# Optimization experiments

Hardware: AMD Instinct MI355X
Metric: run time of the kernel (lower is better)

## Reference

```python
import jax, jax.numpy as jnp
import numpy as np

B, S, D = 4, 1024, 1024
NH, HD = 16, 64            # heads, head_dim
R = 4                      # channel_shrink_ratio
LD, LHD = D // R, HD // R  # layout hidden, layout head_dim
MAXP = 2048                # max_position_embeddings


def _heads(x, nh, hd):
    # [B,S,nh*hd] -> [B,nh,S,hd]
    b, s, _ = x.shape
    return x.reshape(b, s, nh, hd).transpose(0, 2, 1, 3)


def setup_inputs() -> dict:
    key = jax.random.key(0)
    ks = jax.random.split(key, 17)
    init = lambda k, shape: jax.random.normal(k, shape, dtype=jnp.float32) * 0.02
    return {
        "hidden_states": init(ks[0], (B, S, D)),
        "layout_inputs": init(ks[1], (B, S, LD)),
        "attention_mask": jnp.zeros((B, 1, 1, S), jnp.float32),
        # text-stream projections (parameterized as x @ W + b, W:[in,out])
        "wq": init(ks[2], (D, D)), "bq": jnp.zeros((D,), jnp.float32),
        "wk": init(ks[3], (D, D)), "bk": jnp.zeros((D,), jnp.float32),
        "wv": init(ks[4], (D, D)), "bv": jnp.zeros((D,), jnp.float32),
        # layout-stream projections
        "lwq": init(ks[5], (LD, LD)), "lbq": jnp.zeros((LD,), jnp.float32),
        "lwk": init(ks[6], (LD, LD)), "lbk": jnp.zeros((LD,), jnp.float32),
        "lwv": init(ks[7], (LD, LD)), "lbv": jnp.zeros((LD,), jnp.float32),
        # relative distance embedding table [2*MAXP-1, HD]
        "dist_emb": init(ks[8], (2 * MAXP - 1, HD)),
    }


def reference(hidden_states, layout_inputs, attention_mask,
              wq, bq, wk, bk, wv, bv,
              lwq, lbq, lwk, lbk, lwv, lbv, dist_emb):
    # projections + head split
    q = _heads(hidden_states @ wq + bq, NH, HD)   # [B,NH,S,HD]
    k = _heads(hidden_states @ wk + bk, NH, HD)
    v = _heads(hidden_states @ wv + bv, NH, HD)
    lq = _heads(layout_inputs @ lwq + lbq, NH, LHD)  # [B,NH,S,LHD]
    lk = _heads(layout_inputs @ lwk + lbk, NH, LHD)
    lv = _heads(layout_inputs @ lwv + lbv, NH, LHD)

    # raw QK^T scores for both streams
    scores = jnp.einsum('bhld,bhrd->bhlr', q, k)        # [B,NH,S,S]
    lscores = jnp.einsum('bhld,bhrd->bhlr', lq, lk)     # [B,NH,S,S]

    # relative_key positional bias on text stream
    idx = jnp.arange(S)[:, None] - jnp.arange(S)[None, :] + (MAXP - 1)  # [S,S]
    pe = dist_emb[idx]                                   # [S,S,HD]
    scores = scores + jnp.einsum('bhld,lrd->bhlr', q, pe)

    # cross-stream score fusion: both streams share the same combined scores
    combined = scores / np.sqrt(HD) + lscores / np.sqrt(LHD) + attention_mask
    probs = jax.nn.softmax(combined, axis=-1)            # dropout_p = 0 (eval)

    ctx = jnp.einsum('bhlr,bhrd->bhld', probs, v)        # [B,NH,S,HD]
    ctx = ctx.transpose(0, 2, 1, 3).reshape(B, S, D)
    lctx = jnp.einsum('bhlr,bhrd->bhld', probs, lv)      # [B,NH,S,LHD]
    lctx = lctx.transpose(0, 2, 1, 3).reshape(B, S, LD)
    return (ctx, lctx)
```

## Files before the change

### kernel.cpp

```cpp
#include <hip/hip_runtime.h>
#include <math.h>

#define S_LEN 1024
#define NHEAD 16
#define HDIM 64
#define LHDIM 16

typedef __bf16 bf16;
typedef bf16 bf16x4 __attribute__((ext_vector_type(4)));
typedef bf16 bf16x8 __attribute__((ext_vector_type(8)));
typedef float f32x4 __attribute__((ext_vector_type(4)));

#define MFMA16(a, b, c) __builtin_amdgcn_mfma_f32_16x16x32_bf16(a, b, c, 0, 0, 0)

__device__ __forceinline__ void gl2lds16(const void* g, void* l)
{
    __builtin_amdgcn_global_load_lds(
        (const __attribute__((address_space(1))) unsigned int*)g,
        (__attribute__((address_space(3))) unsigned int*)l,
        16, 0, 0);
}

__global__ __launch_bounds__(256)
void prep_kernel(const float* __restrict__ hs,   bf16* __restrict__ hsb,
                 const float* __restrict__ lin,  bf16* __restrict__ linb,
                 const float* __restrict__ de32, bf16* __restrict__ de,
                 const float* __restrict__ W0, const float* __restrict__ W1,
                 const float* __restrict__ W2,
                 bf16* __restrict__ T0, bf16* __restrict__ T1, bf16* __restrict__ T2,
                 const float* __restrict__ LW0, const float* __restrict__ LW1,
                 const float* __restrict__ LW2,
                 bf16* __restrict__ LT0, bf16* __restrict__ LT1, bf16* __restrict__ LT2)
{
    const int bx = blockIdx.x;
    const int t  = threadIdx.x;

    if (bx < 5376) {
        const float* in; bf16* out; int i; int n4;
        if (bx < 4096)      { in = hs;   out = hsb;  i = bx * 256 + t;          n4 = 1048576; }
        else if (bx < 5120) { in = lin;  out = linb; i = (bx - 4096) * 256 + t; n4 = 262144; }
        else                { in = de32; out = de;   i = (bx - 5120) * 256 + t; n4 = 65520; }
        if (i < n4) {
            float4 v = *(const float4*)&in[(size_t)i * 4];
            bf16x4 o = { (bf16)v.x, (bf16)v.y, (bf16)v.z, (bf16)v.w };
            *(bf16x4*)&out[(size_t)i * 4] = o;
        }
        return;
    }

    const int bt = bx - 5376;
    const float* W; bf16* T; int K, N, k0, n0;
    if (bt < 768) {
        int proj = bt >> 8, tile = bt & 255;
        W = proj == 0 ? W0 : (proj == 1 ? W1 : W2);
        T = proj == 0 ? T0 : (proj == 1 ? T1 : T2);
        K = N = 1024; k0 = (tile >> 4) << 6; n0 = (tile & 15) << 6;
    } else {
        int b2 = bt - 768;
        int proj = b2 >> 4, tile = b2 & 15;
        W = proj == 0 ? LW0 : (proj == 1 ? LW1 : LW2);
        T = proj == 0 ? LT0 : (proj == 1 ? LT1 : LT2);
        K = N = 256; k0 = (tile >> 2) << 6; n0 = (tile & 3) << 6;
    }

    __shared__ float Ts[64][65];
    #pragma unroll
    for (int p = 0; p < 4; p++) {
        int li = p * 256 + t;
        int r  = li >> 4, c4 = (li & 15) << 2;
        float4 v = *(const float4*)&W[(size_t)(k0 + r) * N + n0 + c4];
        Ts[r][c4 + 0] = v.x; Ts[r][c4 + 1] = v.y;
        Ts[r][c4 + 2] = v.z; Ts[r][c4 + 3] = v.w;
    }
    __syncthreads();

    int r2 = t >> 2, ks = (t & 3) << 4;
    bf16x8 o0, o1;
    #pragma unroll
    for (int u = 0; u < 8; u++) o0[u] = (bf16)Ts[ks + u][r2];
    #pragma unroll
    for (int u = 0; u < 8; u++) o1[u] = (bf16)Ts[ks + 8 + u][r2];
    *(bf16x8*)&T[(size_t)(n0 + r2) * K + k0 + ks]     = o0;
    *(bf16x8*)&T[(size_t)(n0 + r2) * K + k0 + ks + 8] = o1;
}

__global__ __launch_bounds__(256, 3)
void projm_all_kernel(const bf16* __restrict__ Xt, const bf16* __restrict__ Xl,
                      const bf16* __restrict__ Wt0, const float* __restrict__ B0,
                      const bf16* __restrict__ Wt1, const float* __restrict__ B1,
                      const bf16* __restrict__ Wt2, const float* __restrict__ B2,
                      const bf16* __restrict__ LWt0, const float* __restrict__ LB0,
                      const bf16* __restrict__ LWt1, const float* __restrict__ LB1,
                      const bf16* __restrict__ LWt2, const float* __restrict__ LB2,
                      bf16* __restrict__ O0, bf16* __restrict__ O1, bf16* __restrict__ O2,
                      bf16* __restrict__ LO0, bf16* __restrict__ LO1, bf16* __restrict__ LO2)
{
    const int z = blockIdx.z;
    const bf16* X; const bf16* Wt; const float* Bi; bf16* O;
    float scale; int KDIM, nshift, n0;
    const int m0 = blockIdx.y << 7;

    if (z < 3) {
        X = Xt; KDIM = 1024; nshift = 6;
        Wt = z == 0 ? Wt0 : (z == 1 ? Wt1 : Wt2);
        Bi = z == 0 ? B0  : (z == 1 ? B1  : B2);
        O  = z == 0 ? O0  : (z == 1 ? O1  : O2);
        scale = z == 0 ? 0.125f : 1.0f;
        n0 = blockIdx.x << 7;
    } else {
        if (blockIdx.x >= 6) return;
        int proj = blockIdx.x >> 1;
        X = Xl; KDIM = 256; nshift = 4;
        Wt = proj == 0 ? LWt0 : (proj == 1 ? LWt1 : LWt2);
        Bi = proj == 0 ? LB0  : (proj == 1 ? LB1  : LB2);
        O  = proj == 0 ? LO0  : (proj == 1 ? LO1  : LO2);
        scale = proj == 0 ? 0.25f : 1.0f;
        n0 = (blockIdx.x & 1) << 7;
    }
    const int nhdm = (1 << nshift) - 1;

    __shared__ bf16 As[128 * 32];
    __shared__ bf16 Bs[128 * 32];

    const int t    = threadIdx.x;
    const int wv   = t >> 6;
    const int l64  = t & 63;
    const int ln   = l64 & 15;
    const int quad = l64 >> 4;
    const int wm   = wv & 1;
    const int wn   = wv >> 1;

    const int arow = l64 >> 2;
    const int koff = (l64 & 3) << 3;

    f32x4 acc[4][4];
    #pragma unroll
    for (int i = 0; i < 4; i++)
        #pragma unroll
        for (int j = 0; j < 4; j++) acc[i][j] = (f32x4)0.0f;

    for (int k0 = 0; k0 < KDIM; k0 += 32) {
        #pragma unroll
        for (int c = 0; c < 2; c++) {
            int g = (c * 4 + wv) << 4;
            gl2lds16(&X [(size_t)(m0 + g + arow) * KDIM + k0 + koff], &As[(c * 4 + wv) * 512]);
            gl2lds16(&Wt[(size_t)(n0 + g + arow) * KDIM + k0 + koff], &Bs[(c * 4 + wv) * 512]);
        }
        __syncthreads();

        bf16x8 af[4], bfv[4];
        #pragma unroll
        for (int mt = 0; mt < 4; mt++)
            af[mt] = *(const bf16x8*)&As[(wm * 64 + mt * 16 + ln) * 32 + quad * 8];
        #pragma unroll
        for (int nt = 0; nt < 4; nt++)
            bfv[nt] = *(const bf16x8*)&Bs[(wn * 64 + nt * 16 + ln) * 32 + quad * 8];
        #pragma unroll
        for (int mt = 0; mt < 4; mt++)
            #pragma unroll
            for (int nt = 0; nt < 4; nt++)
                acc[mt][nt] = MFMA16(af[mt], bfv[nt], acc[mt][nt]);
        __syncthreads();
    }

    #pragma unroll
    for (int nt = 0; nt < 4; nt++) {
        int n  = n0 + wn * 64 + nt * 16 + ln;
        float bia = Bi[n];
        int hh = n >> nshift;
        int dd = n & nhdm;
        #pragma unroll
        for (int mt = 0; mt < 4; mt++) {
            #pragma unroll
            for (int reg = 0; reg < 4; reg++) {
                int m  = m0 + wm * 64 + mt * 16 + quad * 4 + reg;
                int bb = m >> 10;
                int s  = m & 1023;
                O[((size_t)((bb * NHEAD + hh) << 10) + s) * (nhdm + 1) + dd] =
                    (bf16)((acc[mt][nt][reg] + bia) * scale);
            }
        }
    }
}

__global__ __launch_bounds__(256, 2)
void attn_kernel(const bf16* __restrict__ qg, const bf16* __restrict__ kg,
                 const bf16* __restrict__ vg, const bf16* __restrict__ lqg,
                 const bf16* __restrict__ lkg, const bf16* __restrict__ lvg,
                 const float* __restrict__ maskg, const bf16* __restrict__ demb,
                 float* __restrict__ octx, float* __restrict__ olctx)
{
    __shared__ bf16 Ks[2][64][104];
    __shared__ bf16 VsT[2][64][72];
    __shared__ bf16 LVsT[2][16][72];
    __shared__ bf16 Ps[128][72];

    const int t    = threadIdx.x;
    const int w    = t >> 6;
    const int lane = t & 63;
    const int ln   = lane & 15;
    const int quad = lane >> 4;
    const int m0   = w << 4;

    const int bh = blockIdx.y;
    const int b  = bh >> 4;
    const int h  = bh & 15;
    const int l0 = blockIdx.x << 7;

    const bf16* qb  = qg  + (size_t)bh * (S_LEN * HDIM);
    const bf16* kb  = kg  + (size_t)bh * (S_LEN * HDIM);
    const bf16* vb  = vg  + (size_t)bh * (S_LEN * HDIM);
    const bf16* lqb = lqg + (size_t)bh * (S_LEN * LHDIM);
    const bf16* lkb = lkg + (size_t)bh * (S_LEN * LHDIM);
    const bf16* lvb = lvg + (size_t)bh * (S_LEN * LHDIM);

    bf16x8 zer, one8;
    #pragma unroll
    for (int u = 0; u < 8; u++) { zer[u] = (bf16)0.0f; one8[u] = (bf16)1.0f; }

    if (t < 128) {
        int row = t >> 1, h8 = (t & 1) << 3;
        *(bf16x8*)&Ks[0][row][80 + h8] = zer;
        *(bf16x8*)&Ks[1][row][80 + h8] = zer;
    }

    bf16x8 af[2][3];
    #pragma unroll
    for (int st = 0; st < 2; st++) {
        const int qrow = l0 + st * 64 + m0 + ln;
        af[st][0] = *(const bf16x8*)&qb[(size_t)qrow * HDIM + quad * 8];
        af[st][1] = *(const bf16x8*)&qb[(size_t)qrow * HDIM + 32 + quad * 8];
        af[st][2] = (quad < 2) ? *(const bf16x8*)&lqb[(size_t)qrow * LHDIM + quad * 8] : zer;
    }

    const int krow = t >> 2, kc8 = (t & 3) << 3;
    const int lkrow = t >> 1, lh8 = (t & 1) << 3;
    const int vr0 = t & 63,  vd80 = (t >> 6) << 3;
    const int vr1 = t & 63,  vd81 = 32 + ((t >> 6) << 3);
    const int lvr = t & 63,  lvd8 = (t >> 6) << 3;

    f32x4 co[2][4];
    f32x4 cl[2];
    f32x4 la[2];
    #pragma unroll
    for (int st = 0; st < 2; st++) {
        #pragma unroll
        for (int i = 0; i < 4; i++) co[st][i] = (f32x4)0.0f;
        cl[st] = (f32x4)0.0f;
        la[st] = (f32x4)0.0f;
    }

    for (int r0 = 0; r0 < S_LEN; r0 += 128) {
        bf16x8 kx[2][2], lkx[2], vx[2][2], lvx[2];
        float msv[2][4];
        #pragma unroll
        for (int sub = 0; sub < 2; sub++) {
            const int rr = r0 + sub * 64;
            kx[sub][0] = *(const bf16x8*)&kb[(size_t)(rr + krow) * HDIM + kc8];
            kx[sub][1] = *(const bf16x8*)&kb[(size_t)(rr + krow) * HDIM + 32 + kc8];
            lkx[sub] = (t < 128) ? *(const bf16x8*)&lkb[(size_t)(rr + lkrow) * LHDIM + lh8] : zer;
            vx[sub][0] = *(const bf16x8*)&vb[(size_t)(rr + vr0) * HDIM + vd80];
            vx[sub][1] = *(const bf16x8*)&vb[(size_t)(rr + vr1) * HDIM + vd81];
            lvx[sub] = (t < 128) ? *(const bf16x8*)&lvb[(size_t)(rr + lvr) * LHDIM + lvd8] : zer;
            #pragma unroll
            for (int nt = 0; nt < 4; nt++)
                msv[sub][nt] = maskg[b * S_LEN + rr + nt * 16 + ln];
        }

        __syncthreads();

        #pragma unroll
        for (int sub = 0; sub < 2; sub++) {
            *(bf16x8*)&Ks[sub][krow][kc8]      = kx[sub][0];
            *(bf16x8*)&Ks[sub][krow][32 + kc8] = kx[sub][1];
            if (t < 128) *(bf16x8*)&Ks[sub][lkrow][64 + lh8] = lkx[sub];
            #pragma unroll
            for (int u = 0; u < 8; u++) VsT[sub][vd80 + u][vr0] = vx[sub][0][u];
            #pragma unroll
            for (int u = 0; u < 8; u++) VsT[sub][vd81 + u][vr1] = vx[sub][1][u];
            if (t < 128) {
                #pragma unroll
                for (int u = 0; u < 8; u++) LVsT[sub][lvd8 + u][lvr] = lvx[sub][u];
            }
        }

        __syncthreads();

        #pragma unroll
        for (int sub = 0; sub < 2; sub++) {
            const int jb = l0 - (r0 + sub * 64) + 1984;

            bf16x8 ef[2][5][2];
            #pragma unroll
            for (int st = 0; st < 2; st++)
                #pragma unroll
                for (int ct = 0; ct < 5; ct++) {
                    const bf16* ep = &demb[(size_t)(jb + st * 64 + m0 + ct * 16 + ln) * HDIM + quad * 8];
                    ef[st][ct][0] = *(const bf16x8*)ep;
                    ef[st][ct][1] = *(const bf16x8*)(ep + 32);
                }

            #pragma unroll
            for (int st = 0; st < 2; st++) {
                const int mb = st * 64 + m0;

                f32x4 hh[5];
                #pragma unroll
                for (int ct = 0; ct < 5; ct++) {
                    hh[ct] = (f32x4)0.0f;
                    hh[ct] = MFMA16(af[st][0], ef[st][ct][0], hh[ct]);
                    hh[ct] = MFMA16(af[st][1], ef[st][ct][1], hh[ct]);
                }

                f32x4 sc[4];
                #pragma unroll
                for (int nt = 0; nt < 4; nt++) {
                    const bf16* kr = &Ks[sub][nt * 16 + ln][quad * 8];
                    sc[nt] = (f32x4)0.0f;
                    sc[nt] = MFMA16(af[st][0], *(const bf16x8*)(kr),      sc[nt]);
                    sc[nt] = MFMA16(af[st][1], *(const bf16x8*)(kr + 32), sc[nt]);
                    sc[nt] = MFMA16(af[st][2], *(const bf16x8*)(kr + 64), sc[nt]);
                }

                float bias[4][4];
                #pragma unroll
                for (int reg = 0; reg < 4; reg++) {
                    int d = quad * 4 + reg - ln + 63;
                    int srcLane = (quad << 4) | (d & 15);
                    float sh[5];
                    #pragma unroll
                    for (int ct = 0; ct < 5; ct++)
                        sh[ct] = __shfl(hh[ct][reg], srcLane);
                    bool f4 = (d >> 4) == 4;
                    #pragma unroll
                    for (int nt = 0; nt < 4; nt++)
                        bias[nt][reg] = f4 ? sh[4 - nt] : sh[3 - nt];
                }

                #pragma unroll
                for (int nt = 0; nt < 4; nt++)
                    #pragma unroll
                    for (int reg = 0; reg < 4; reg++) {
                        float p = __expf(sc[nt][reg] + bias[nt][reg] + msv[sub][nt]);
                        Ps[mb + quad * 4 + reg][nt * 16 + ln] = (bf16)p;
                    }

                #pragma unroll
                for (int ks = 0; ks < 2; ks++) {
                    bf16x8 ap = *(const bf16x8*)&Ps[mb + ln][ks * 32 + quad * 8];
                    cl[st] = MFMA16(ap, *(const bf16x8*)&LVsT[sub][ln][ks * 32 + quad * 8], cl[st]);
                    la[st] = MFMA16(ap, one8, la[st]);
                    #pragma unroll
                    for (int nt = 0; nt < 4; nt++)
                        co[st][nt] = MFMA16(ap,
                                            *(const bf16x8*)&VsT[sub][nt * 16 + ln][ks * 32 + quad * 8],
                                            co[st][nt]);
                }
            }
        }
    }

    #pragma unroll
    for (int st = 0; st < 2; st++)
        #pragma unroll
        for (int reg = 0; reg < 4; reg++) {
            int s = l0 + st * 64 + m0 + quad * 4 + reg;
            float inv = 1.0f / la[st][reg];
            #pragma unroll
            for (int nt = 0; nt < 4; nt++)
                octx[(size_t)(b * S_LEN + s) * 1024 + h * 64 + nt * 16 + ln] = co[st][nt][reg] * inv;
            olctx[(size_t)(b * S_LEN + s) * 256 + h * 16 + ln] = cl[st][reg] * inv;
        }
}

extern "C" void kernel_launch(void* const* d_in, const int* in_sizes, int n_in,
                              void* d_out, int out_size, void* d_ws, size_t ws_size,
                              hipStream_t stream)
{
    (void)in_sizes; (void)n_in; (void)out_size; (void)ws_size;

    const float* hs   = (const float*)d_in[0];
    const float* lin  = (const float*)d_in[1];
    const float* mask = (const float*)d_in[2];
    const float* wq  = (const float*)d_in[3];  const float* bq  = (const float*)d_in[4];
    const float* wk  = (const float*)d_in[5];  const float* bk  = (const float*)d_in[6];
    const float* wv  = (const float*)d_in[7];  const float* bv  = (const float*)d_in[8];
    const float* lwq = (const float*)d_in[9];  const float* lbq = (const float*)d_in[10];
    const float* lwk = (const float*)d_in[11]; const float* lbk = (const float*)d_in[12];
    const float* lwv = (const float*)d_in[13]; const float* lbv = (const float*)d_in[14];
    const float* demb = (const float*)d_in[15];

    bf16* ws = (bf16*)d_ws;
    bf16* q    = ws;
    bf16* k    = ws + 4194304;
    bf16* v    = ws + 8388608;
    bf16* lq   = ws + 12582912;
    bf16* lk   = ws + 13631488;
    bf16* lv   = ws + 14680064;
    bf16* de   = ws + 15728640;
    bf16* hsb  = ws + 16000000;
    bf16* linb = ws + 20194304;
    bf16* wqt  = ws + 21242880;
    bf16* wkt  = ws + 22291456;
    bf16* wvt  = ws + 23340032;
    bf16* lwqt = ws + 24388608;
    bf16* lwkt = ws + 24454144;
    bf16* lwvt = ws + 24519680;

    prep_kernel<<<dim3(6192), 256, 0, stream>>>(
        hs, hsb, lin, linb, demb, de,
        wq, wk, wv, wqt, wkt, wvt, lwq, lwk, lwv, lwqt, lwkt, lwvt);

    projm_all_kernel<<<dim3(8, 32, 4), 256, 0, stream>>>(
        hsb, linb,
        wqt, bq, wkt, bk, wvt, bv,
        lwqt, lbq, lwkt, lbk, lwvt, lbv,
        q, k, v, lq, lk, lv);

    float* octx  = (float*)d_out;
    float* olctx = (float*)d_out + 4194304;
    attn_kernel<<<dim3(8, 64), 256, 0, stream>>>(
        q, k, v, lq, lk, lv, mask, de, octx, olctx);
}
```

Baseline: 235.7 us.

## Use 512 threads per attention block with one 16-row strip per wave

The attention kernel moves from 4 waves each handling two 16-row query strips to 8 waves each handling a single strip, so per-thread accumulators, Q fragments and distance-embedding fragments are halved. K/V staging loads are redistributed across the 512 threads. The aim is lower register pressure and more resident waves per CU to hide latency, at the cost of more threads contending on barriers and shared-memory staging per tile.

After: 238.6 us. No clear change (+1.2%).

```diff
diff --git a/kernel.cpp b/kernel.cpp
--- a/kernel.cpp
+++ b/kernel.cpp
@@ -183,7 +183,7 @@
     }
 }
 
-__global__ __launch_bounds__(256, 2)
+__global__ __launch_bounds__(512, 4)
 void attn_kernel(const bf16* __restrict__ qg, const bf16* __restrict__ kg,
                  const bf16* __restrict__ vg, const bf16* __restrict__ lqg,
                  const bf16* __restrict__ lkg, const bf16* __restrict__ lvg,
@@ -200,7 +200,7 @@
     const int lane = t & 63;
     const int ln   = lane & 15;
     const int quad = lane >> 4;
-    const int m0   = w << 4;
+    const int mb   = w << 4;
 
     const int bh = blockIdx.y;
     const int b  = bh >> 4;
@@ -224,43 +224,34 @@
         *(bf16x8*)&Ks[1][row][80 + h8] = zer;
     }
 
-    bf16x8 af[2][3];
-    #pragma unroll
-    for (int st = 0; st < 2; st++) {
-        const int qrow = l0 + st * 64 + m0 + ln;
-        af[st][0] = *(const bf16x8*)&qb[(size_t)qrow * HDIM + quad * 8];
-        af[st][1] = *(const bf16x8*)&qb[(size_t)qrow * HDIM + 32 + quad * 8];
-        af[st][2] = (quad < 2) ? *(const bf16x8*)&lqb[(size_t)qrow * LHDIM + quad * 8] : zer;
-    }
-
-    const int krow = t >> 2, kc8 = (t & 3) << 3;
+    const int qrow = l0 + mb + ln;
+    bf16x8 af[3];
+    af[0] = *(const bf16x8*)&qb[(size_t)qrow * HDIM + quad * 8];
+    af[1] = *(const bf16x8*)&qb[(size_t)qrow * HDIM + 32 + quad * 8];
+    af[2] = (quad < 2) ? *(const bf16x8*)&lqb[(size_t)qrow * LHDIM + quad * 8] : zer;
+
+    const int krow = t >> 3, kc8 = (t & 7) << 3;
     const int lkrow = t >> 1, lh8 = (t & 1) << 3;
-    const int vr0 = t & 63,  vd80 = (t >> 6) << 3;
-    const int vr1 = t & 63,  vd81 = 32 + ((t >> 6) << 3);
-    const int lvr = t & 63,  lvd8 = (t >> 6) << 3;
-
-    f32x4 co[2][4];
-    f32x4 cl[2];
-    f32x4 la[2];
-    #pragma unroll
-    for (int st = 0; st < 2; st++) {
-        #pragma unroll
-        for (int i = 0; i < 4; i++) co[st][i] = (f32x4)0.0f;
-        cl[st] = (f32x4)0.0f;
-        la[st] = (f32x4)0.0f;
-    }
+    const int vr = t & 63,  vd8 = (t >> 6) << 3;
+    const int lvr = t & 63, lvd8 = ((t >> 6) & 1) << 3;
+
+    f32x4 co[4];
+    f32x4 cl;
+    f32x4 la;
+    #pragma unroll
+    for (int i = 0; i < 4; i++) co[i] = (f32x4)0.0f;
+    cl = (f32x4)0.0f;
+    la = (f32x4)0.0f;
 
     for (int r0 = 0; r0 < S_LEN; r0 += 128) {
-        bf16x8 kx[2][2], lkx[2], vx[2][2], lvx[2];
+        bf16x8 kx[2], lkx[2], vx[2], lvx[2];
         float msv[2][4];
         #pragma unroll
         for (int sub = 0; sub < 2; sub++) {
             const int rr = r0 + sub * 64;
-            kx[sub][0] = *(const bf16x8*)&kb[(size_t)(rr + krow) * HDIM + kc8];
-            kx[sub][1] = *(const bf16x8*)&kb[(size_t)(rr + krow) * HDIM + 32 + kc8];
+            kx[sub]  = *(const bf16x8*)&kb[(size_t)(rr + krow) * HDIM + kc8];
             lkx[sub] = (t < 128) ? *(const bf16x8*)&lkb[(size_t)(rr + lkrow) * LHDIM + lh8] : zer;
-            vx[sub][0] = *(const bf16x8*)&vb[(size_t)(rr + vr0) * HDIM + vd80];
-            vx[sub][1] = *(const bf16x8*)&vb[(size_t)(rr + vr1) * HDIM + vd81];
+            vx[sub]  = *(const bf16x8*)&vb[(size_t)(rr + vr) * HDIM + vd8];
             lvx[sub] = (t < 128) ? *(const bf16x8*)&lvb[(size_t)(rr + lvr) * LHDIM + lvd8] : zer;
             #pragma unroll
             for (int nt = 0; nt < 4; nt++)
@@ -271,13 +262,10 @@
 
         #pragma unroll
         for (int sub = 0; sub < 2; sub++) {
-            *(bf16x8*)&Ks[sub][krow][kc8]      = kx[sub][0];
-            *(bf16x8*)&Ks[sub][krow][32 + kc8] = kx[sub][1];
+            *(bf16x8*)&Ks[sub][krow][kc8] = kx[sub];
             if (t < 128) *(bf16x8*)&Ks[sub][lkrow][64 + lh8] = lkx[sub];
             #pragma unroll
-            for (int u = 0; u < 8; u++) VsT[sub][vd80 + u][vr0] = vx[sub][0][u];
-            #pragma unroll
-            for (int u = 0; u < 8; u++) VsT[sub][vd81 + u][vr1] = vx[sub][1][u];
+            for (int u = 0; u < 8; u++) VsT[sub][vd8 + u][vr] = vx[sub][u];
             if (t < 128) {
                 #pragma unroll
                 for (int u = 0; u < 8; u++) LVsT[sub][lvd8 + u][lvr] = lvx[sub][u];
@@ -290,87 +278,78 @@
         for (int sub = 0; sub < 2; sub++) {
             const int jb = l0 - (r0 + sub * 64) + 1984;
 
-            bf16x8 ef[2][5][2];
-            #pragma unroll
-            for (int st = 0; st < 2; st++)
+            bf16x8 ef[5][2];
+            #pragma unroll
+            for (int ct = 0; ct < 5; ct++) {
+                const bf16* ep = &demb[(size_t)(jb + mb + ct * 16 + ln) * HDIM + quad * 8];
+                ef[ct][0] = *(const bf16x8*)ep;
+                ef[ct][1] = *(const bf16x8*)(ep + 32);
+            }
+
+            f32x4 hh[5];
+            #pragma unroll
+            for (int ct = 0; ct < 5; ct++) {
+                hh[ct] = (f32x4)0.0f;
+                hh[ct] = MFMA16(af[0], ef[ct][0], hh[ct]);
+                hh[ct] = MFMA16(af[1], ef[ct][1], hh[ct]);
+            }
+
+            f32x4 sc[4];
+            #pragma unroll
+            for (int nt = 0; nt < 4; nt++) {
+                const bf16* kr = &Ks[sub][nt * 16 + ln][quad * 8];
+                sc[nt] = (f32x4)0.0f;
+                sc[nt] = MFMA16(af[0], *(const bf16x8*)(kr),      sc[nt]);
+                sc[nt] = MFMA16(af[1], *(const bf16x8*)(kr + 32), sc[nt]);
+                sc[nt] = MFMA16(af[2], *(const bf16x8*)(kr + 64), sc[nt]);
+            }
+
+            float bias[4][4];
+            #pragma unroll
+            for (int reg = 0; reg < 4; reg++) {
+                int d = quad * 4 + reg - ln + 63;
+                int srcLane = (quad << 4) | (d & 15);
+                float sh[5];
                 #pragma unroll
-                for (int ct = 0; ct < 5; ct++) {
-                    const bf16* ep = &demb[(size_t)(jb + st * 64 + m0 + ct * 16 + ln) * HDIM + quad * 8];
-                    ef[st][ct][0] = *(const bf16x8*)ep;
-                    ef[st][ct][1] = *(const bf16x8*)(ep + 32);
-                }
-
-            #pragma unroll
-            for (int st = 0; st < 2; st++) {
-                const int mb = st * 64 + m0;
-
-                f32x4 hh[5];
+                for (int ct = 0; ct < 5; ct++)
+                    sh[ct] = __shfl(hh[ct][reg], srcLane);
+                bool f4 = (d >> 4) == 4;
                 #pragma unroll
-                for (int ct = 0; ct < 5; ct++) {
-                    hh[ct] = (f32x4)0.0f;
-                    hh[ct] = MFMA16(af[st][0], ef[st][ct][0], hh[ct]);
-                    hh[ct] = MFMA16(af[st][1], ef[st][ct][1], hh[ct]);
-                }
-
-                f32x4 sc[4];
-                #pragma unroll
-                for (int nt = 0; nt < 4; nt++) {
-                    const bf16* kr = &Ks[sub][nt * 16 + ln][quad * 8];
-                    sc[nt] = (f32x4)0.0f;
-                    sc[nt] = MFMA16(af[st][0], *(const bf16x8*)(kr),      sc[nt]);
-                    sc[nt] = MFMA16(af[st][1], *(const bf16x8*)(kr + 32), sc[nt]);
-                    sc[nt] = MFMA16(af[st][2], *(const bf16x8*)(kr + 64), sc[nt]);
-                }
-
-                float bias[4][4];
+                for (int nt = 0; nt < 4; nt++)
+                    bias[nt][reg] = f4 ? sh[4 - nt] : sh[3 - nt];
+            }
+
+            #pragma unroll
+            for (int nt = 0; nt < 4; nt++)
                 #pragma unroll
                 for (int reg = 0; reg < 4; reg++) {
-                    int d = quad * 4 + reg - ln + 63;
-                    int srcLane = (quad << 4) | (d & 15);
-                    float sh[5];
-                    #pragma unroll
-                    for (int ct = 0; ct < 5; ct++)
-                        sh[ct] = __shfl(hh[ct][reg], srcLane);
-                    bool f4 = (d >> 4) == 4;
-                    #pragma unroll
-                    for (int nt = 0; nt < 4; nt++)
-                        bias[nt][reg] = f4 ? sh[4 - nt] : sh[3 - nt];
+                    float p = __expf(sc[nt][reg] + bias[nt][reg] + msv[sub][nt]);
+                    Ps[mb + quad * 4 + reg][nt * 16 + ln] = (bf16)p;
                 }
 
+            #pragma unroll
+            for (int ks = 0; ks < 2; ks++) {
+                bf16x8 ap = *(const bf16x8*)&Ps[mb + ln][ks * 32 + quad * 8];
+                cl = MFMA16(ap, *(const bf16x8*)&LVsT[sub][ln][ks * 32 + quad * 8], cl);
+                la = MFMA16(ap, one8, la);
                 #pragma unroll
                 for (int nt = 0; nt < 4; nt++)
-                    #pragma unroll
-                    for (int reg = 0; reg < 4; reg++) {
-                        float p = __expf(sc[nt][reg] + bias[nt][reg] + msv[sub][nt]);
-                        Ps[mb + quad * 4 + reg][nt * 16 + ln] = (bf16)p;
-                    }
-
-                #pragma unroll
-                for (int ks = 0; ks < 2; ks++) {
-                    bf16x8 ap = *(const bf16x8*)&Ps[mb + ln][ks * 32 + quad * 8];
-                    cl[st] = MFMA16(ap, *(const bf16x8*)&LVsT[sub][ln][ks * 32 + quad * 8], cl[st]);
-                    la[st] = MFMA16(ap, one8, la[st]);
-                    #pragma unroll
-                    for (int nt = 0; nt < 4; nt++)
-                        co[st][nt] = MFMA16(ap,
-                                            *(const bf16x8*)&VsT[sub][nt * 16 + ln][ks * 32 + quad * 8],
-                                            co[st][nt]);
-                }
-            }
-        }
-    }
-
-    #pragma unroll
-    for (int st = 0; st < 2; st++)
-        #pragma unroll
-        for (int reg = 0; reg < 4; reg++) {
-            int s = l0 + st * 64 + m0 + quad * 4 + reg;
-            float inv = 1.0f / la[st][reg];
-            #pragma unroll
-            for (int nt = 0; nt < 4; nt++)
-                octx[(size_t)(b * S_LEN + s) * 1024 + h * 64 + nt * 16 + ln] = co[st][nt][reg] * inv;
-            olctx[(size_t)(b * S_LEN + s) * 256 + h * 16 + ln] = cl[st][reg] * inv;
-        }
+                    co[nt] = MFMA16(ap,
+                                    *(const bf16x8*)&VsT[sub][nt * 16 + ln][ks * 32 + quad * 8],
+                                    co[nt]);
+            }
+        }
+    }
+
+    #pragma unroll
+    for (int reg = 0; reg < 4; reg++) {
+        int s = l0 + mb + quad * 4 + reg;
+        float inv = 1.0f / la[reg];
+        #pragma unroll
+        for (int nt = 0; nt < 4; nt++)
+            octx[(size_t)(b * S_LEN + s) * 1024 + h * 64 + nt * 16 + ln] = co[nt][reg] * inv;
+        olctx[(size_t)(b * S_LEN + s) * 256 + h * 16 + ln] = cl[reg] * inv;
+    }
 }
 
 extern "C" void kernel_launch(void* const* d_in, const int* in_sizes, int n_in,
@@ -419,6 +398,6 @@
 
     float* octx  = (float*)d_out;
     float* olctx = (float*)d_out + 4194304;
-    attn_kernel<<<dim3(8, 64), 256, 0, stream>>>(
+    attn_kernel<<<dim3(8, 64), 512, 0, stream>>>(
         q, k, v, lq, lk, lv, mask, de, octx, olctx);
 }
```

## Enlarge attention blocks to 256 query rows with 8 waves and reuse fragments

Applied to the files above, without the earlier changes.

The attention kernel now runs 512-thread blocks covering 256 query rows, with each wave owning two adjacent 16-row tiles. This halves the number of K/V tile loads per query row and lets the two tiles share overlapping distance-embedding fragments (6 loads instead of 10). K, V and LV fragments are read from LDS once per sub-tile into registers and reused across both row tiles. The grid becomes 1D with a swizzled block-to-(batch, head, tile) mapping, likely aimed at L2 locality. The cost is higher register pressure and fewer, larger blocks (256), which may reduce occupancy and latency hiding.

Result: faster. 210.8 us (-10.6%).

```diff
diff --git a/kernel.cpp b/kernel.cpp
--- a/kernel.cpp
+++ b/kernel.cpp
@@ -183,7 +183,7 @@
     }
 }
 
-__global__ __launch_bounds__(256, 2)
+__global__ __launch_bounds__(512, 2)
 void attn_kernel(const bf16* __restrict__ qg, const bf16* __restrict__ kg,
                  const bf16* __restrict__ vg, const bf16* __restrict__ lqg,
                  const bf16* __restrict__ lkg, const bf16* __restrict__ lvg,
@@ -193,19 +193,21 @@
     __shared__ bf16 Ks[2][64][104];
     __shared__ bf16 VsT[2][64][72];
     __shared__ bf16 LVsT[2][16][72];
-    __shared__ bf16 Ps[128][72];
+    __shared__ bf16 Ps[256][72];
 
     const int t    = threadIdx.x;
     const int w    = t >> 6;
     const int lane = t & 63;
     const int ln   = lane & 15;
     const int quad = lane >> 4;
-    const int m0   = w << 4;
-
-    const int bh = blockIdx.y;
-    const int b  = bh >> 4;
-    const int h  = bh & 15;
-    const int l0 = blockIdx.x << 7;
+    const int mb0  = w << 5;
+
+    const int lid = blockIdx.x;
+    const int bh  = (lid & 7) * 8 + (lid >> 5);
+    const int xt  = (lid >> 3) & 3;
+    const int b   = bh >> 4;
+    const int h   = bh & 15;
+    const int l0  = xt << 8;
 
     const bf16* qb  = qg  + (size_t)bh * (S_LEN * HDIM);
     const bf16* kb  = kg  + (size_t)bh * (S_LEN * HDIM);
@@ -227,17 +229,16 @@
     bf16x8 af[2][3];
     #pragma unroll
     for (int st = 0; st < 2; st++) {
-        const int qrow = l0 + st * 64 + m0 + ln;
+        const int qrow = l0 + mb0 + st * 16 + ln;
         af[st][0] = *(const bf16x8*)&qb[(size_t)qrow * HDIM + quad * 8];
         af[st][1] = *(const bf16x8*)&qb[(size_t)qrow * HDIM + 32 + quad * 8];
         af[st][2] = (quad < 2) ? *(const bf16x8*)&lqb[(size_t)qrow * LHDIM + quad * 8] : zer;
     }
 
-    const int krow = t >> 2, kc8 = (t & 3) << 3;
+    const int krow = t >> 3, kc8 = (t & 7) << 3;
     const int lkrow = t >> 1, lh8 = (t & 1) << 3;
-    const int vr0 = t & 63,  vd80 = (t >> 6) << 3;
-    const int vr1 = t & 63,  vd81 = 32 + ((t >> 6) << 3);
-    const int lvr = t & 63,  lvd8 = (t >> 6) << 3;
+    const int vr = t & 63,  vd8 = w << 3;
+    const int lvr = t & 63, lvd8 = (w & 1) << 3;
 
     f32x4 co[2][4];
     f32x4 cl[2];
@@ -251,16 +252,14 @@
     }
 
     for (int r0 = 0; r0 < S_LEN; r0 += 128) {
-        bf16x8 kx[2][2], lkx[2], vx[2][2], lvx[2];
+        bf16x8 kx[2], lkx[2], vx[2], lvx[2];
         float msv[2][4];
         #pragma unroll
         for (int sub = 0; sub < 2; sub++) {
             const int rr = r0 + sub * 64;
-            kx[sub][0] = *(const bf16x8*)&kb[(size_t)(rr + krow) * HDIM + kc8];
-            kx[sub][1] = *(const bf16x8*)&kb[(size_t)(rr + krow) * HDIM + 32 + kc8];
+            kx[sub]  = *(const bf16x8*)&kb[(size_t)(rr + krow) * HDIM + kc8];
             lkx[sub] = (t < 128) ? *(const bf16x8*)&lkb[(size_t)(rr + lkrow) * LHDIM + lh8] : zer;
-            vx[sub][0] = *(const bf16x8*)&vb[(size_t)(rr + vr0) * HDIM + vd80];
-            vx[sub][1] = *(const bf16x8*)&vb[(size_t)(rr + vr1) * HDIM + vd81];
+            vx[sub]  = *(const bf16x8*)&vb[(size_t)(rr + vr) * HDIM + vd8];
             lvx[sub] = (t < 128) ? *(const bf16x8*)&lvb[(size_t)(rr + lvr) * LHDIM + lvd8] : zer;
             #pragma unroll
             for (int nt = 0; nt < 4; nt++)
@@ -271,13 +270,10 @@
 
         #pragma unroll
         for (int sub = 0; sub < 2; sub++) {
-            *(bf16x8*)&Ks[sub][krow][kc8]      = kx[sub][0];
-            *(bf16x8*)&Ks[sub][krow][32 + kc8] = kx[sub][1];
+            *(bf16x8*)&Ks[sub][krow][kc8] = kx[sub];
             if (t < 128) *(bf16x8*)&Ks[sub][lkrow][64 + lh8] = lkx[sub];
             #pragma unroll
-            for (int u = 0; u < 8; u++) VsT[sub][vd80 + u][vr0] = vx[sub][0][u];
-            #pragma unroll
-            for (int u = 0; u < 8; u++) VsT[sub][vd81 + u][vr1] = vx[sub][1][u];
+            for (int u = 0; u < 8; u++) VsT[sub][vd8 + u][vr] = vx[sub][u];
             if (t < 128) {
                 #pragma unroll
                 for (int u = 0; u < 8; u++) LVsT[sub][lvd8 + u][lvr] = lvx[sub][u];
@@ -290,36 +286,42 @@
         for (int sub = 0; sub < 2; sub++) {
             const int jb = l0 - (r0 + sub * 64) + 1984;
 
-            bf16x8 ef[2][5][2];
-            #pragma unroll
-            for (int st = 0; st < 2; st++)
-                #pragma unroll
-                for (int ct = 0; ct < 5; ct++) {
-                    const bf16* ep = &demb[(size_t)(jb + st * 64 + m0 + ct * 16 + ln) * HDIM + quad * 8];
-                    ef[st][ct][0] = *(const bf16x8*)ep;
-                    ef[st][ct][1] = *(const bf16x8*)(ep + 32);
-                }
+            bf16x8 ef[6][2];
+            #pragma unroll
+            for (int ct2 = 0; ct2 < 6; ct2++) {
+                const bf16* ep = &demb[(size_t)(jb + mb0 + ct2 * 16 + ln) * HDIM + quad * 8];
+                ef[ct2][0] = *(const bf16x8*)ep;
+                ef[ct2][1] = *(const bf16x8*)(ep + 32);
+            }
+
+            bf16x8 kf[4][3];
+            #pragma unroll
+            for (int nt = 0; nt < 4; nt++) {
+                const bf16* kr = &Ks[sub][nt * 16 + ln][quad * 8];
+                kf[nt][0] = *(const bf16x8*)(kr);
+                kf[nt][1] = *(const bf16x8*)(kr + 32);
+                kf[nt][2] = *(const bf16x8*)(kr + 64);
+            }
 
             #pragma unroll
             for (int st = 0; st < 2; st++) {
-                const int mb = st * 64 + m0;
+                const int mq = mb0 + st * 16;
 
                 f32x4 hh[5];
                 #pragma unroll
                 for (int ct = 0; ct < 5; ct++) {
                     hh[ct] = (f32x4)0.0f;
-                    hh[ct] = MFMA16(af[st][0], ef[st][ct][0], hh[ct]);
-                    hh[ct] = MFMA16(af[st][1], ef[st][ct][1], hh[ct]);
+                    hh[ct] = MFMA16(af[st][0], ef[st + ct][0], hh[ct]);
+                    hh[ct] = MFMA16(af[st][1], ef[st + ct][1], hh[ct]);
                 }
 
                 f32x4 sc[4];
                 #pragma unroll
                 for (int nt = 0; nt < 4; nt++) {
-                    const bf16* kr = &Ks[sub][nt * 16 + ln][quad * 8];
                     sc[nt] = (f32x4)0.0f;
-                    sc[nt] = MFMA16(af[st][0], *(const bf16x8*)(kr),      sc[nt]);
-                    sc[nt] = MFMA16(af[st][1], *(const bf16x8*)(kr + 32), sc[nt]);
-                    sc[nt] = MFMA16(af[st][2], *(const bf16x8*)(kr + 64), sc[nt]);
+                    sc[nt] = MFMA16(af[st][0], kf[nt][0], sc[nt]);
+                    sc[nt] = MFMA16(af[st][1], kf[nt][1], sc[nt]);
+                    sc[nt] = MFMA16(af[st][2], kf[nt][2], sc[nt]);
                 }
 
                 float bias[4][4];
@@ -342,19 +344,30 @@
                     #pragma unroll
                     for (int reg = 0; reg < 4; reg++) {
                         float p = __expf(sc[nt][reg] + bias[nt][reg] + msv[sub][nt]);
-                        Ps[mb + quad * 4 + reg][nt * 16 + ln] = (bf16)p;
+                        Ps[mq + quad * 4 + reg][nt * 16 + ln] = (bf16)p;
                     }
-
+            }
+
+            bf16x8 vf[4][2], lvf[2];
+            #pragma unroll
+            for (int ks = 0; ks < 2; ks++) {
+                #pragma unroll
+                for (int nt = 0; nt < 4; nt++)
+                    vf[nt][ks] = *(const bf16x8*)&VsT[sub][nt * 16 + ln][ks * 32 + quad * 8];
+                lvf[ks] = *(const bf16x8*)&LVsT[sub][ln][ks * 32 + quad * 8];
+            }
+
+            #pragma unroll
+            for (int st = 0; st < 2; st++) {
+                const int mq = mb0 + st * 16;
                 #pragma unroll
                 for (int ks = 0; ks < 2; ks++) {
-                    bf16x8 ap = *(const bf16x8*)&Ps[mb + ln][ks * 32 + quad * 8];
-                    cl[st] = MFMA16(ap, *(const bf16x8*)&LVsT[sub][ln][ks * 32 + quad * 8], cl[st]);
+                    bf16x8 ap = *(const bf16x8*)&Ps[mq + ln][ks * 32 + quad * 8];
+                    cl[st] = MFMA16(ap, lvf[ks], cl[st]);
                     la[st] = MFMA16(ap, one8, la[st]);
                     #pragma unroll
                     for (int nt = 0; nt < 4; nt++)
-                        co[st][nt] = MFMA16(ap,
-                                            *(const bf16x8*)&VsT[sub][nt * 16 + ln][ks * 32 + quad * 8],
-                                            co[st][nt]);
+                        co[st][nt] = MFMA16(ap, vf[nt][ks], co[st][nt]);
                 }
             }
         }
@@ -364,7 +377,7 @@
     for (int st = 0; st < 2; st++)
         #pragma unroll
         for (int reg = 0; reg < 4; reg++) {
-            int s = l0 + st * 64 + m0 + quad * 4 + reg;
+            int s = l0 + mb0 + st * 16 + quad * 4 + reg;
             float inv = 1.0f / la[st][reg];
             #pragma unroll
             for (int nt = 0; nt < 4; nt++)
@@ -419,6 +432,6 @@
 
     float* octx  = (float*)d_out;
     float* olctx = (float*)d_out + 4194304;
-    attn_kernel<<<dim3(8, 64), 256, 0, stream>>>(
+    attn_kernel<<<dim3(256), 512, 0, stream>>>(
         q, k, v, lq, lk, lv, mask, de, octx, olctx);
 }
```
